# Kernel optimization log

Measured on AMD Instinct MI355X. Metric: run time of the kernel, lower is better.

The kernel has to match this reference:

```python
import jax, jax.numpy as jnp
import numpy as np

B, T, D, H = 64, 512, 768, 96


def setup_inputs() -> dict:
    key = jax.random.key(0)
    kx, kq, kk, kv = jax.random.split(key, 4)
    x = jax.random.normal(kx, (B, T, D), dtype=jnp.float32)
    # Linear weights stored as [in, out]; scaled like torch default init
    s = 1.0 / np.sqrt(D)
    Wq = jax.random.normal(kq, (D, H), dtype=jnp.float32) * s
    Wk = jax.random.normal(kk, (D, H), dtype=jnp.float32) * s
    Wv = jax.random.normal(kv, (D, H), dtype=jnp.float32) * s
    return {"x": x, "Wq": Wq, "Wk": Wk, "Wv": Wv}


def reference(x, Wq, Wk, Wv):
    # q,k,v: [B,T,H]
    q = jnp.einsum('btd,dh->bth', x, Wq)
    k = jnp.einsum('btd,dh->bth', x, Wk)
    v = jnp.einsum('btd,dh->bth', x, Wv)
    scale = 1.0 / jnp.sqrt(jnp.array(q.shape[-1], dtype=x.dtype))
    # scores: [B,T,T]
    wei = jnp.einsum('bqh,bkh->bqk', q, k) * scale
    causal = jnp.tril(jnp.ones((T, T), dtype=bool))
    wei = jnp.where(causal, wei, jnp.array(-jnp.inf, dtype=wei.dtype))
    attn = jax.nn.softmax(wei, axis=-1)
    return jnp.einsum('bqk,bkh->bqh', attn, v)
```

## Files before the change

### kernel.cpp

```cpp
#include <hip/hip_runtime.h>
#include <hip/hip_bf16.h>
#include <math.h>

#define B_ 64
#define T_ 512
#define D_ 768
#define H_ 96
#define M_ (B_*T_)

typedef __attribute__((ext_vector_type(8))) short short8;
typedef __attribute__((ext_vector_type(4))) float f32x4;

__device__ __forceinline__ short f2bf(float f) {
  unsigned u = __float_as_uint(f);
  unsigned r = (u + 0x7FFFu + ((u >> 16) & 1u)) >> 16;
  return (short)r;
}

__device__ __forceinline__ void gl16(const void* g, void* l) {
  __builtin_amdgcn_global_load_lds(
      (const __attribute__((address_space(1))) unsigned*)g,
      (__attribute__((address_space(3))) unsigned*)l, 16, 0, 0);
}

__global__ __launch_bounds__(256) void wt_kernel(
    const float* __restrict__ Wq, const float* __restrict__ Wk,
    const float* __restrict__ Wv, short* __restrict__ wt)
{
  int id = blockIdx.x * 256 + threadIdx.x;
  if (id >= 3*H_*D_) return;
  int n = id % 288;
  int k = id / 288;
  int mi = n / 96, cc = n % 96;
  const float* Wm = (mi == 0) ? Wq : ((mi == 1) ? Wk : Wv);
  wt[(size_t)n * D_ + k] = f2bf(Wm[(size_t)k * H_ + cc]);
}

#define BKP 32

__global__ __launch_bounds__(256) void qkv_mfma_kernel(
    const float* __restrict__ x, const short* __restrict__ wt,
    short* __restrict__ qb, short* __restrict__ kb, short* __restrict__ vb)
{
  __shared__ float As[2][64][32];
  __shared__ short Bs[2][288][32];

  const int t    = threadIdx.x;
  const int row0 = blockIdx.x * 64;
  const int lane = t & 63;
  const int w    = t >> 6;
  const int l15  = lane & 15;
  const int l4   = lane >> 4;

  auto stageA = [&](int buf, int k0) {
    #pragma unroll
    for (int i = 0; i < 2; ++i) {
      int inst = w * 2 + i;
      int row  = inst * 8 + (lane >> 3);
      int c16  = (lane & 7) ^ ((lane >> 3) & 7);
      const char* g = (const char*)(x + (size_t)(row0 + row) * D_ + k0) + c16 * 16;
      char* l = (char*)&As[buf][0][0] + inst * 1024 + lane * 16;
      gl16(g, l);
    }
  };
  auto stageB = [&](int buf, int k0) {
    #pragma unroll
    for (int i = 0; i < 5; ++i) {
      int inst = w + 4 * i;
      if (inst < 18) {
        int row = inst * 16 + (lane >> 2);
        int c16 = (lane & 3) ^ ((lane >> 2) & 3);
        const char* g = (const char*)(wt + (size_t)row * D_ + k0) + c16 * 16;
        char* l = (char*)&Bs[buf][0][0] + inst * 1024 + lane * 16;
        gl16(g, l);
      }
    }
  };

  f32x4 acc[18];
  #pragma unroll
  for (int ci = 0; ci < 18; ++ci) acc[ci] = (f32x4){0.f, 0.f, 0.f, 0.f};

  stageA(0, 0);
  stageB(0, 0);
  __syncthreads();

  const int arow = w * 16 + l15;
  const char* Abase = (const char*)&As[0][0][0];
  const char* Bbase = (const char*)&Bs[0][0][0];

  for (int ks = 0; ks < 24; ++ks) {
    int buf = ks & 1;
    if (ks + 1 < 24) { stageA(buf ^ 1, (ks + 1) * BKP); stageB(buf ^ 1, (ks + 1) * BKP); }

    const char* ab = Abase + (size_t)buf * 8192 + arow * 128;
    float4 a0 = *reinterpret_cast<const float4*>(ab + (((l4 * 2 + 0) ^ (arow & 7)) * 16));
    float4 a1 = *reinterpret_cast<const float4*>(ab + (((l4 * 2 + 1) ^ (arow & 7)) * 16));
    short8 af;
    af[0] = f2bf(a0.x); af[1] = f2bf(a0.y); af[2] = f2bf(a0.z); af[3] = f2bf(a0.w);
    af[4] = f2bf(a1.x); af[5] = f2bf(a1.y); af[6] = f2bf(a1.z); af[7] = f2bf(a1.w);

    #pragma unroll
    for (int ci = 0; ci < 18; ++ci) {
      int brow = ci * 16 + l15;
      short8 bf = *reinterpret_cast<const short8*>(
          Bbase + (size_t)buf * 18432 + brow * 64 + ((l4 ^ (brow & 3)) * 16));
      acc[ci] = __builtin_amdgcn_mfma_f32_16x16x32_bf16(af, bf, acc[ci], 0, 0, 0);
    }
    __syncthreads();
  }

  const int rbase = row0 + w * 16 + l4 * 4;
  #pragma unroll
  for (int ci = 0; ci < 18; ++ci) {
    int mi = ci / 6;
    int cc = (ci % 6) * 16 + l15;
    short* Om = (mi == 0) ? qb : ((mi == 1) ? kb : vb);
    #pragma unroll
    for (int reg = 0; reg < 4; ++reg)
      Om[(size_t)(rbase + reg) * H_ + cc] = f2bf(acc[ci][reg]);
  }
}

#define QB 32
#define KVB 32
#define KSTR 104
#define VSTR 40
#define PSTR 40

__global__ __launch_bounds__(128) void attn_mfma_kernel(
    const short* __restrict__ qb, const short* __restrict__ kb,
    const short* __restrict__ vb, float* __restrict__ out)
{
  __shared__ short ks[KVB][KSTR];
  __shared__ short vs[H_][VSTR];
  __shared__ short ps[2][16][PSTR];

  const int t    = threadIdx.x;
  const int lane = t & 63;
  const int w    = t >> 6;
  const int l15  = lane & 15;
  const int l4   = lane >> 4;
  const int qi   = 15 - blockIdx.x;
  const int b    = blockIdx.y;
  const int q0   = qi * QB;

  short8 qf[3];
  {
    const short* qbase = qb + ((size_t)(b * T_) + q0 + w * 16 + l15) * H_;
    #pragma unroll
    for (int f = 0; f < 3; ++f)
      qf[f] = *reinterpret_cast<const short8*>(qbase + f * 32 + l4 * 8);
  }

  f32x4 acc[6];
  #pragma unroll
  for (int c = 0; c < 6; ++c) acc[c] = (f32x4){0.f, 0.f, 0.f, 0.f};
  float m_r[4] = {-INFINITY, -INFINITY, -INFINITY, -INFINITY};
  float l_r[4] = {0.f, 0.f, 0.f, 0.f};
  const float scale = 0.10206207261596576f;

  const int jmax = q0 + QB;
  for (int j0 = 0; j0 < jmax; j0 += KVB) {
    __syncthreads();
    {
      int row = t >> 2, seg = t & 3;
      const short* src = kb + ((size_t)(b * T_) + j0 + row) * H_ + seg * 24;
      short* dst = &ks[row][seg * 24];
      *reinterpret_cast<short8*>(dst)      = *reinterpret_cast<const short8*>(src);
      *reinterpret_cast<short8*>(dst + 8)  = *reinterpret_cast<const short8*>(src + 8);
      *reinterpret_cast<short8*>(dst + 16) = *reinterpret_cast<const short8*>(src + 16);
    }
    {
      #pragma unroll
      for (int i = 0; i < 3; ++i) {
        int c = t + i * 128;
        int tok = c / 12;
        int m   = c % 12;
        int h0  = m * 8;
        short8 v = *reinterpret_cast<const short8*>(
            vb + (size_t)(b * T_ + j0 + tok) * H_ + h0);
        int tokS = tok ^ ((m & 3) << 3);
        #pragma unroll
        for (int j = 0; j < 8; ++j) vs[h0 + j][tokS] = v[j];
      }
    }
    __syncthreads();

    f32x4 sfr[2];
    sfr[0] = (f32x4){0.f,0.f,0.f,0.f};
    sfr[1] = (f32x4){0.f,0.f,0.f,0.f};
    #pragma unroll
    for (int ct = 0; ct < 2; ++ct)
      #pragma unroll
      for (int f = 0; f < 3; ++f) {
        short8 kf = *reinterpret_cast<const short8*>(&ks[ct * 16 + l15][f * 32 + l4 * 8]);
        sfr[ct] = __builtin_amdgcn_mfma_f32_16x16x32_bf16(qf[f], kf, sfr[ct], 0, 0, 0);
      }

    const int qrow = q0 + w * 16 + l4 * 4;
    float p0[4], p1[4], fsc[4];
    #pragma unroll
    for (int reg = 0; reg < 4; ++reg) {
      float s0 = sfr[0][reg] * scale;
      float s1 = sfr[1][reg] * scale;
      if (j0 + l15      > qrow + reg) s0 = -INFINITY;
      if (j0 + l15 + 16 > qrow + reg) s1 = -INFINITY;
      float tm = fmaxf(s0, s1);
      #pragma unroll
      for (int o = 1; o < 16; o <<= 1) tm = fmaxf(tm, __shfl_xor(tm, o));
      float Mnew = fmaxf(m_r[reg], tm);
      p0[reg] = __expf(s0 - Mnew);
      p1[reg] = __expf(s1 - Mnew);
      float psum = p0[reg] + p1[reg];
      #pragma unroll
      for (int o = 1; o < 16; o <<= 1) psum += __shfl_xor(psum, o);
      fsc[reg] = __expf(m_r[reg] - Mnew);
      m_r[reg] = Mnew;
      l_r[reg] = l_r[reg] * fsc[reg] + psum;
    }
    #pragma unroll
    for (int c = 0; c < 6; ++c)
      #pragma unroll
      for (int reg = 0; reg < 4; ++reg) acc[c][reg] *= fsc[reg];

    #pragma unroll
    for (int reg = 0; reg < 4; ++reg) {
      ps[w][l4 * 4 + reg][l15]      = f2bf(p0[reg]);
      ps[w][l4 * 4 + reg][l15 + 16] = f2bf(p1[reg]);
    }
    short8 pa = *reinterpret_cast<const short8*>(&ps[w][l15][l4 * 8]);

    #pragma unroll
    for (int c = 0; c < 6; ++c) {
      int h = c * 16 + l15;
      short8 vf = *reinterpret_cast<const short8*>(
          &vs[h][(l4 ^ ((h >> 3) & 3)) * 8]);
      acc[c] = __builtin_amdgcn_mfma_f32_16x16x32_bf16(pa, vf, acc[c], 0, 0, 0);
    }
  }

  float inv[4];
  #pragma unroll
  for (int reg = 0; reg < 4; ++reg) inv[reg] = 1.f / l_r[reg];
  #pragma unroll
  for (int c = 0; c < 6; ++c) {
    #pragma unroll
    for (int reg = 0; reg < 4; ++reg) {
      size_t row = (size_t)(b * T_) + q0 + w * 16 + l4 * 4 + reg;
      out[row * H_ + c * 16 + l15] = acc[c][reg] * inv[reg];
    }
  }
}

extern "C" void kernel_launch(void* const* d_in, const int* in_sizes, int n_in,
                              void* d_out, int out_size, void* d_ws, size_t ws_size,
                              hipStream_t stream) {
  const float* x  = (const float*)d_in[0];
  const float* Wq = (const float*)d_in[1];
  const float* Wk = (const float*)d_in[2];
  const float* Wv = (const float*)d_in[3];

  short* wt = (short*)d_ws;
  short* qb = (short*)((char*)d_ws + 524288);
  short* kb = qb + (size_t)M_ * H_;
  short* vb = kb + (size_t)M_ * H_;
  float* outp = (float*)d_out;

  hipLaunchKernelGGL(wt_kernel, dim3((3*H_*D_ + 255)/256), dim3(256), 0, stream,
                     Wq, Wk, Wv, wt);
  hipLaunchKernelGGL(qkv_mfma_kernel, dim3(M_/64), dim3(256), 0, stream,
                     x, wt, qb, kb, vb);
  hipLaunchKernelGGL(attn_mfma_kernel, dim3(T_/QB, B_), dim3(128), 0, stream,
                     qb, kb, vb, outp);
}
```

Measured before the change: 81.52 us.

## Restructure QKV projection into persistent column-group blocks with LDS-resident weights

The QKV projection kernel is reorganized so that each block owns a 48-column slice of the fused weight matrix and loads that whole slice (all K) into LDS once. A persistent grid of 6x85 blocks then loops over 32-row strips of x, with each wave streaming x directly from global memory into registers through a 3-deep software prefetch and converting it to bf16 before the MFMAs. This removes the per-k-step shared-memory staging and barriers for x and the repeated weight reloads. In exchange, x is now read six times, once per column group, instead of once, and per-wave register pressure and latency hiding now depend on the register prefetch.

```diff
diff --git a/kernel.cpp b/kernel.cpp
--- a/kernel.cpp
+++ b/kernel.cpp
@@ -15,12 +15,6 @@
   unsigned u = __float_as_uint(f);
   unsigned r = (u + 0x7FFFu + ((u >> 16) & 1u)) >> 16;
   return (short)r;
-}
-
-__device__ __forceinline__ void gl16(const void* g, void* l) {
-  __builtin_amdgcn_global_load_lds(
-      (const __attribute__((address_space(1))) unsigned*)g,
-      (__attribute__((address_space(3))) unsigned*)l, 16, 0, 0);
 }
 
 __global__ __launch_bounds__(256) void wt_kernel(
@@ -36,89 +30,95 @@
   wt[(size_t)n * D_ + k] = f2bf(Wm[(size_t)k * H_ + cc]);
 }
 
-#define BKP 32
+#define NGRP 6
+#define BPG  85
 
 __global__ __launch_bounds__(256) void qkv_mfma_kernel(
     const float* __restrict__ x, const short* __restrict__ wt,
     short* __restrict__ qb, short* __restrict__ kb, short* __restrict__ vb)
 {
-  __shared__ float As[2][64][32];
-  __shared__ short Bs[2][288][32];
+  __shared__ short8 Bs[3 * 24 * 64];
 
   const int t    = threadIdx.x;
-  const int row0 = blockIdx.x * 64;
   const int lane = t & 63;
   const int w    = t >> 6;
   const int l15  = lane & 15;
   const int l4   = lane >> 4;
-
-  auto stageA = [&](int buf, int k0) {
-    #pragma unroll
-    for (int i = 0; i < 2; ++i) {
-      int inst = w * 2 + i;
-      int row  = inst * 8 + (lane >> 3);
-      int c16  = (lane & 7) ^ ((lane >> 3) & 7);
-      const char* g = (const char*)(x + (size_t)(row0 + row) * D_ + k0) + c16 * 16;
-      char* l = (char*)&As[buf][0][0] + inst * 1024 + lane * 16;
-      gl16(g, l);
-    }
-  };
-  auto stageB = [&](int buf, int k0) {
-    #pragma unroll
-    for (int i = 0; i < 5; ++i) {
-      int inst = w + 4 * i;
-      if (inst < 18) {
-        int row = inst * 16 + (lane >> 2);
-        int c16 = (lane & 3) ^ ((lane >> 2) & 3);
-        const char* g = (const char*)(wt + (size_t)row * D_ + k0) + c16 * 16;
-        char* l = (char*)&Bs[buf][0][0] + inst * 1024 + lane * 16;
-        gl16(g, l);
-      }
-    }
-  };
-
-  f32x4 acc[18];
-  #pragma unroll
-  for (int ci = 0; ci < 18; ++ci) acc[ci] = (f32x4){0.f, 0.f, 0.f, 0.f};
-
-  stageA(0, 0);
-  stageB(0, 0);
+  const int cg   = blockIdx.x / BPG;
+  const int bg   = blockIdx.x % BPG;
+
+  for (int idx = t; idx < 3 * 24 * 64; idx += 256) {
+    int lidx = idx & 63;
+    int ks   = (idx >> 6) % 24;
+    int ci   = idx / (24 * 64);
+    int row  = cg * 48 + ci * 16 + (lidx & 15);
+    int k    = ks * 32 + (lidx >> 4) * 8;
+    Bs[idx] = *reinterpret_cast<const short8*>(wt + (size_t)row * D_ + k);
+  }
   __syncthreads();
 
-  const int arow = w * 16 + l15;
-  const char* Abase = (const char*)&As[0][0][0];
-  const char* Bbase = (const char*)&Bs[0][0][0];
-
-  for (int ks = 0; ks < 24; ++ks) {
-    int buf = ks & 1;
-    if (ks + 1 < 24) { stageA(buf ^ 1, (ks + 1) * BKP); stageB(buf ^ 1, (ks + 1) * BKP); }
-
-    const char* ab = Abase + (size_t)buf * 8192 + arow * 128;
-    float4 a0 = *reinterpret_cast<const float4*>(ab + (((l4 * 2 + 0) ^ (arow & 7)) * 16));
-    float4 a1 = *reinterpret_cast<const float4*>(ab + (((l4 * 2 + 1) ^ (arow & 7)) * 16));
-    short8 af;
-    af[0] = f2bf(a0.x); af[1] = f2bf(a0.y); af[2] = f2bf(a0.z); af[3] = f2bf(a0.w);
-    af[4] = f2bf(a1.x); af[5] = f2bf(a1.y); af[6] = f2bf(a1.z); af[7] = f2bf(a1.w);
-
-    #pragma unroll
-    for (int ci = 0; ci < 18; ++ci) {
-      int brow = ci * 16 + l15;
-      short8 bf = *reinterpret_cast<const short8*>(
-          Bbase + (size_t)buf * 18432 + brow * 64 + ((l4 ^ (brow & 3)) * 16));
-      acc[ci] = __builtin_amdgcn_mfma_f32_16x16x32_bf16(af, bf, acc[ci], 0, 0, 0);
-    }
-    __syncthreads();
-  }
-
-  const int rbase = row0 + w * 16 + l4 * 4;
-  #pragma unroll
-  for (int ci = 0; ci < 18; ++ci) {
-    int mi = ci / 6;
-    int cc = (ci % 6) * 16 + l15;
-    short* Om = (mi == 0) ? qb : ((mi == 1) ? kb : vb);
-    #pragma unroll
-    for (int reg = 0; reg < 4; ++reg)
-      Om[(size_t)(rbase + reg) * H_ + cc] = f2bf(acc[ci][reg]);
+  const int gw = bg * 4 + w;
+  const int mi = cg >> 1;
+  const int c0 = (cg & 1) * 48;
+  short* Om = (mi == 0) ? qb : ((mi == 1) ? kb : vb);
+
+  for (int s = gw; s < 1024; s += 340) {
+    const int r0 = s * 32;
+    const float* xr0 = x + (size_t)(r0 + l15) * D_ + l4 * 8;
+    const float* xr1 = x + (size_t)(r0 + 16 + l15) * D_ + l4 * 8;
+
+    f32x4 acc[2][3];
+    #pragma unroll
+    for (int ri = 0; ri < 2; ++ri)
+      #pragma unroll
+      for (int ci = 0; ci < 3; ++ci) acc[ri][ci] = (f32x4){0.f, 0.f, 0.f, 0.f};
+
+    float4 p[3][4];
+    #pragma unroll
+    for (int j = 0; j < 3; ++j) {
+      p[j][0] = *reinterpret_cast<const float4*>(xr0 + j * 32);
+      p[j][1] = *reinterpret_cast<const float4*>(xr0 + j * 32 + 4);
+      p[j][2] = *reinterpret_cast<const float4*>(xr1 + j * 32);
+      p[j][3] = *reinterpret_cast<const float4*>(xr1 + j * 32 + 4);
+    }
+
+    #pragma unroll
+    for (int ks = 0; ks < 24; ++ks) {
+      const int slot = ks % 3;
+      short8 af0, af1;
+      af0[0] = f2bf(p[slot][0].x); af0[1] = f2bf(p[slot][0].y);
+      af0[2] = f2bf(p[slot][0].z); af0[3] = f2bf(p[slot][0].w);
+      af0[4] = f2bf(p[slot][1].x); af0[5] = f2bf(p[slot][1].y);
+      af0[6] = f2bf(p[slot][1].z); af0[7] = f2bf(p[slot][1].w);
+      af1[0] = f2bf(p[slot][2].x); af1[1] = f2bf(p[slot][2].y);
+      af1[2] = f2bf(p[slot][2].z); af1[3] = f2bf(p[slot][2].w);
+      af1[4] = f2bf(p[slot][3].x); af1[5] = f2bf(p[slot][3].y);
+      af1[6] = f2bf(p[slot][3].z); af1[7] = f2bf(p[slot][3].w);
+      if (ks + 3 < 24) {
+        p[slot][0] = *reinterpret_cast<const float4*>(xr0 + (ks + 3) * 32);
+        p[slot][1] = *reinterpret_cast<const float4*>(xr0 + (ks + 3) * 32 + 4);
+        p[slot][2] = *reinterpret_cast<const float4*>(xr1 + (ks + 3) * 32);
+        p[slot][3] = *reinterpret_cast<const float4*>(xr1 + (ks + 3) * 32 + 4);
+      }
+      #pragma unroll
+      for (int ci = 0; ci < 3; ++ci) {
+        short8 bf = Bs[(ci * 24 + ks) * 64 + lane];
+        acc[0][ci] = __builtin_amdgcn_mfma_f32_16x16x32_bf16(af0, bf, acc[0][ci], 0, 0, 0);
+        acc[1][ci] = __builtin_amdgcn_mfma_f32_16x16x32_bf16(af1, bf, acc[1][ci], 0, 0, 0);
+      }
+    }
+
+    #pragma unroll
+    for (int ri = 0; ri < 2; ++ri) {
+      int rbase = r0 + ri * 16 + l4 * 4;
+      #pragma unroll
+      for (int ci = 0; ci < 3; ++ci) {
+        int cc = c0 + ci * 16 + l15;
+        #pragma unroll
+        for (int reg = 0; reg < 4; ++reg)
+          Om[(size_t)(rbase + reg) * H_ + cc] = f2bf(acc[ri][ci][reg]);
+      }
+    }
   }
 }
 
@@ -269,7 +269,7 @@
 
   hipLaunchKernelGGL(wt_kernel, dim3((3*H_*D_ + 255)/256), dim3(256), 0, stream,
                      Wq, Wk, Wv, wt);
-  hipLaunchKernelGGL(qkv_mfma_kernel, dim3(M_/64), dim3(256), 0, stream,
+  hipLaunchKernelGGL(qkv_mfma_kernel, dim3(NGRP * BPG), dim3(256), 0, stream,
                      x, wt, qb, kb, vb);
   hipLaunchKernelGGL(attn_mfma_kernel, dim3(T_/QB, B_), dim3(128), 0, stream,
                      qb, kb, vb, outp);
```

Result: slower. 207.9 us (+155.0%).

## Enlarge QKV GEMM tile to 128 rows with 2x2 warp grid and triple-buffered LDS

Applied to the files above, without the earlier changes.

The QKV projection kernel now processes 128 rows per block, with warps arranged 2x2 so each warp computes a 64x144 sub-tile with 4x9 MFMA accumulators. This reuses each A and B fragment across more MFMAs, which cuts LDS reads per MFMA and halves the number of blocks that reload the weight matrix. Staging moves to a three-buffer ring with explicit vmcnt waits and raw barriers, so two k-slices are in flight at once. In exchange, register pressure rises (144 accumulator floats), LDS use grows to about 104KB, and launch_bounds(256,1) caps occupancy at one block per CU.

```diff
diff --git a/kernel.cpp b/kernel.cpp
--- a/kernel.cpp
+++ b/kernel.cpp
@@ -36,89 +36,112 @@
   wt[(size_t)n * D_ + k] = f2bf(Wm[(size_t)k * H_ + cc]);
 }
 
+#define BMP 128
 #define BKP 32
-
-__global__ __launch_bounds__(256) void qkv_mfma_kernel(
+#define ABYTES 16384
+#define BBYTES 18432
+#define BUFB (ABYTES + BBYTES)
+
+__global__ __launch_bounds__(256, 1) void qkv_mfma_kernel(
     const float* __restrict__ x, const short* __restrict__ wt,
     short* __restrict__ qb, short* __restrict__ kb, short* __restrict__ vb)
 {
-  __shared__ float As[2][64][32];
-  __shared__ short Bs[2][288][32];
+  __shared__ char LDS[3][BUFB];
 
   const int t    = threadIdx.x;
-  const int row0 = blockIdx.x * 64;
+  const int row0 = blockIdx.x * BMP;
   const int lane = t & 63;
   const int w    = t >> 6;
+  const int wr   = w >> 1;
+  const int wc   = w & 1;
   const int l15  = lane & 15;
   const int l4   = lane >> 4;
 
-  auto stageA = [&](int buf, int k0) {
-    #pragma unroll
-    for (int i = 0; i < 2; ++i) {
-      int inst = w * 2 + i;
-      int row  = inst * 8 + (lane >> 3);
-      int c16  = (lane & 7) ^ ((lane >> 3) & 7);
-      const char* g = (const char*)(x + (size_t)(row0 + row) * D_ + k0) + c16 * 16;
-      char* l = (char*)&As[buf][0][0] + inst * 1024 + lane * 16;
-      gl16(g, l);
+  auto stage = [&](char* base, int k0) {
+    #pragma unroll
+    for (int i = 0; i < 9; ++i) {
+      int slot = w * 9 + i;
+      if (slot < 16) {
+        int inst = slot;
+        int row  = inst * 8 + (lane >> 3);
+        int c16  = (lane & 7) ^ ((lane >> 3) & 7);
+        const char* g = (const char*)(x + (size_t)(row0 + row) * D_ + k0) + c16 * 16;
+        gl16(g, base + inst * 1024 + lane * 16);
+      } else {
+        int inst = (slot < 34) ? (slot - 16) : (slot - 34);
+        int row  = inst * 16 + (lane >> 2);
+        int c16  = (lane & 3) ^ ((lane >> 2) & 3);
+        const char* g = (const char*)(wt + (size_t)row * D_ + k0) + c16 * 16;
+        gl16(g, base + ABYTES + inst * 1024 + lane * 16);
+      }
     }
   };
-  auto stageB = [&](int buf, int k0) {
-    #pragma unroll
-    for (int i = 0; i < 5; ++i) {
-      int inst = w + 4 * i;
-      if (inst < 18) {
-        int row = inst * 16 + (lane >> 2);
-        int c16 = (lane & 3) ^ ((lane >> 2) & 3);
-        const char* g = (const char*)(wt + (size_t)row * D_ + k0) + c16 * 16;
-        char* l = (char*)&Bs[buf][0][0] + inst * 1024 + lane * 16;
-        gl16(g, l);
-      }
+
+  f32x4 acc[4][9];
+  #pragma unroll
+  for (int ri = 0; ri < 4; ++ri)
+    #pragma unroll
+    for (int ci = 0; ci < 9; ++ci) acc[ri][ci] = (f32x4){0.f, 0.f, 0.f, 0.f};
+
+  auto compute = [&](const char* base) {
+    short8 af[4];
+    #pragma unroll
+    for (int ri = 0; ri < 4; ++ri) {
+      int arow = wr * 64 + ri * 16 + l15;
+      const char* ab = base + arow * 128;
+      float4 a0 = *reinterpret_cast<const float4*>(ab + (((l4 * 2 + 0) ^ (arow & 7)) * 16));
+      float4 a1 = *reinterpret_cast<const float4*>(ab + (((l4 * 2 + 1) ^ (arow & 7)) * 16));
+      short8 v;
+      v[0] = f2bf(a0.x); v[1] = f2bf(a0.y); v[2] = f2bf(a0.z); v[3] = f2bf(a0.w);
+      v[4] = f2bf(a1.x); v[5] = f2bf(a1.y); v[6] = f2bf(a1.z); v[7] = f2bf(a1.w);
+      af[ri] = v;
+    }
+    #pragma unroll
+    for (int ci = 0; ci < 9; ++ci) {
+      int brow = wc * 144 + ci * 16 + l15;
+      short8 bf = *reinterpret_cast<const short8*>(
+          base + ABYTES + brow * 64 + ((l4 ^ (brow & 3)) * 16));
+      #pragma unroll
+      for (int ri = 0; ri < 4; ++ri)
+        acc[ri][ci] = __builtin_amdgcn_mfma_f32_16x16x32_bf16(af[ri], bf, acc[ri][ci], 0, 0, 0);
     }
   };
 
-  f32x4 acc[18];
-  #pragma unroll
-  for (int ci = 0; ci < 18; ++ci) acc[ci] = (f32x4){0.f, 0.f, 0.f, 0.f};
-
-  stageA(0, 0);
-  stageB(0, 0);
-  __syncthreads();
-
-  const int arow = w * 16 + l15;
-  const char* Abase = (const char*)&As[0][0][0];
-  const char* Bbase = (const char*)&Bs[0][0][0];
-
-  for (int ks = 0; ks < 24; ++ks) {
-    int buf = ks & 1;
-    if (ks + 1 < 24) { stageA(buf ^ 1, (ks + 1) * BKP); stageB(buf ^ 1, (ks + 1) * BKP); }
-
-    const char* ab = Abase + (size_t)buf * 8192 + arow * 128;
-    float4 a0 = *reinterpret_cast<const float4*>(ab + (((l4 * 2 + 0) ^ (arow & 7)) * 16));
-    float4 a1 = *reinterpret_cast<const float4*>(ab + (((l4 * 2 + 1) ^ (arow & 7)) * 16));
-    short8 af;
-    af[0] = f2bf(a0.x); af[1] = f2bf(a0.y); af[2] = f2bf(a0.z); af[3] = f2bf(a0.w);
-    af[4] = f2bf(a1.x); af[5] = f2bf(a1.y); af[6] = f2bf(a1.z); af[7] = f2bf(a1.w);
-
-    #pragma unroll
-    for (int ci = 0; ci < 18; ++ci) {
-      int brow = ci * 16 + l15;
-      short8 bf = *reinterpret_cast<const short8*>(
-          Bbase + (size_t)buf * 18432 + brow * 64 + ((l4 ^ (brow & 3)) * 16));
-      acc[ci] = __builtin_amdgcn_mfma_f32_16x16x32_bf16(af, bf, acc[ci], 0, 0, 0);
-    }
-    __syncthreads();
-  }
-
-  const int rbase = row0 + w * 16 + l4 * 4;
-  #pragma unroll
-  for (int ci = 0; ci < 18; ++ci) {
-    int mi = ci / 6;
-    int cc = (ci % 6) * 16 + l15;
+  char* b0 = &LDS[0][0];
+  char* b1 = &LDS[1][0];
+  char* b2 = &LDS[2][0];
+
+  stage(b0, 0);
+  stage(b1, BKP);
+
+  for (int ks = 0; ks < 22; ++ks) {
+    stage(b2, (ks + 2) * BKP);
+    asm volatile("s_waitcnt vmcnt(18)" ::: "memory");
+    asm volatile("s_barrier" ::: "memory");
+    compute(b0);
+    asm volatile("s_barrier" ::: "memory");
+    char* tmp = b0; b0 = b1; b1 = b2; b2 = tmp;
+  }
+  asm volatile("s_waitcnt vmcnt(9)" ::: "memory");
+  asm volatile("s_barrier" ::: "memory");
+  compute(b0);
+  asm volatile("s_waitcnt vmcnt(0)" ::: "memory");
+  asm volatile("s_barrier" ::: "memory");
+  compute(b1);
+
+  #pragma unroll
+  for (int ci = 0; ci < 9; ++ci) {
+    int ncol = wc * 144 + ci * 16;
+    int mi   = ncol / 96;
+    int cc   = ncol % 96 + l15;
     short* Om = (mi == 0) ? qb : ((mi == 1) ? kb : vb);
     #pragma unroll
-    for (int reg = 0; reg < 4; ++reg)
-      Om[(size_t)(rbase + reg) * H_ + cc] = f2bf(acc[ci][reg]);
+    for (int ri = 0; ri < 4; ++ri) {
+      int rbase = row0 + wr * 64 + ri * 16 + l4 * 4;
+      #pragma unroll
+      for (int reg = 0; reg < 4; ++reg)
+        Om[(size_t)(rbase + reg) * H_ + cc] = f2bf(acc[ri][ci][reg]);
+    }
   }
 }
 
@@ -269,7 +292,7 @@
 
   hipLaunchKernelGGL(wt_kernel, dim3((3*H_*D_ + 255)/256), dim3(256), 0, stream,
                      Wq, Wk, Wv, wt);
-  hipLaunchKernelGGL(qkv_mfma_kernel, dim3(M_/64), dim3(256), 0, stream,
+  hipLaunchKernelGGL(qkv_mfma_kernel, dim3(M_/BMP), dim3(256), 0, stream,
                      x, wt, qb, kb, vb);
   hipLaunchKernelGGL(attn_mfma_kernel, dim3(T_/QB, B_), dim3(128), 0, stream,
                      qb, kb, vb, outp);
```

Result: slower. 91.72 us (+12.5%).
